# Kernel tuning notes

Hardware: AMD Instinct MI355X
Metric: run time of the kernel (lower is better)

Reference implementation:

```python
import jax, jax.numpy as jnp
import numpy as np

EPS = 1e-15
MAX_ATANH = 1.0 - 1e-5
V = 2097152   # total nodes (B*N*L flattened)
E = 8388608   # edges, ~avg degree 4 (temporal + parent/child)
ATT = 16
MAXD = 512    # mixer embedding table size
# curvature c = 1.0 (registered buffer, constant)


def _mobius_add(a, b):
    # Poincare ball Mobius addition, c = 1
    a2 = jnp.sum(a * a, -1, keepdims=True)
    b2 = jnp.sum(b * b, -1, keepdims=True)
    ab = jnp.sum(a * b, -1, keepdims=True)
    num = (1.0 + 2.0 * ab + b2) * a + (1.0 - a2) * b
    den = 1.0 + 2.0 * ab + a2 * b2
    return num / jnp.maximum(den, EPS)


def _log_map_x(x, y):
    # log_x(y): tangent vector at x pointing to y (c = 1)
    sub = _mobius_add(-x, y)
    n = jnp.maximum(jnp.linalg.norm(sub, axis=-1, keepdims=True), EPS)
    lam = 2.0 / jnp.maximum(1.0 - jnp.sum(x * x, -1, keepdims=True), EPS)
    return (2.0 / lam) * jnp.arctanh(jnp.minimum(n, MAX_ATANH)) * (sub / n)


def _exp_map_x(x, v):
    # exp_x(v) (c = 1)
    n = jnp.maximum(jnp.linalg.norm(v, axis=-1, keepdims=True), EPS)
    lam = 2.0 / jnp.maximum(1.0 - jnp.sum(x * x, -1, keepdims=True), EPS)
    return _mobius_add(x, jnp.tanh(0.5 * lam * n) * (v / n))


def setup_inputs() -> dict:
    key = jax.random.key(0)
    ks = jax.random.split(key, 8)
    # node embeddings strictly inside the unit ball: exp0 of a small tangent vec
    v0 = 0.5 * jax.random.normal(ks[0], (V, 2), jnp.float32)
    n0 = jnp.maximum(jnp.linalg.norm(v0, axis=-1, keepdims=True), EPS)
    x = jnp.tanh(n0) * v0 / n0
    edge_index = jax.random.randint(ks[1], (2, E), 0, V)
    depth = jax.random.randint(ks[2], (V,), 0, MAXD)
    W1 = jax.random.normal(ks[3], (2, ATT), jnp.float32) / jnp.sqrt(2.0)
    b1 = 0.1 * jax.random.normal(ks[4], (ATT,), jnp.float32)
    W2 = jax.random.normal(ks[5], (ATT, 1), jnp.float32) / jnp.sqrt(float(ATT))
    eta = jnp.float32(1.0)
    depth_scale = 1.0 + 0.01 * jax.random.normal(ks[6], (MAXD,), jnp.float32)
    depth_theta = 0.01 * jax.random.normal(ks[7], (MAXD,), jnp.float32)
    return {"x": x, "W1": W1, "b1": b1, "W2": W2, "eta": eta,
            "depth_scale": depth_scale, "depth_theta": depth_theta,
            "edge_index": edge_index, "depth": depth}


def reference(x, W1, b1, W2, eta, depth_scale, depth_theta, edge_index, depth):
    row, col = edge_index[0], edge_index[1]
    xi = x[row]                      # [E,2] gather target endpoints
    xj = x[col]                      # [E,2] gather source endpoints
    v_ij = _log_map_x(xi, xj)        # [E,2] hyperbolic log-map
    # small per-edge MLP scorer: Linear(2,16) -> GELU(exact) -> Linear(16,1)
    h = jax.nn.gelu(v_ij @ W1 + b1, approximate=False)
    scores = (h @ W2)[:, 0]          # [E]
    # segment softmax over target node (row)
    mx = jax.ops.segment_max(scores, row, num_segments=V)
    e = jnp.exp(scores - mx[row])
    den = jax.ops.segment_sum(e, row, num_segments=V)
    alpha = e / jnp.maximum(den[row], EPS)
    # scatter-add aggregate in tangent space
    m = jax.ops.segment_sum(alpha[:, None] * v_ij, row, num_segments=V)  # [V,2]
    # depth-gated mixer: per-node scale + 2D rotation
    d = jnp.minimum(depth, MAXD - 1)
    k = depth_scale[d][:, None]
    ang = depth_theta[d]
    ca, sa = jnp.cos(ang), jnp.sin(ang)
    m = k * jnp.stack([ca * m[:, 0] - sa * m[:, 1],
                       sa * m[:, 0] + ca * m[:, 1]], axis=-1)
    # exp-map update
    return _exp_map_x(x, eta * m)
```

## Files before the change

### kernel.cpp

```cpp
#include <hip/hip_runtime.h>
#include <math.h>

#define EPSF 1e-15f
#define MAX_ATANH (1.0f - 1e-5f)
#define ATT 16

#define LOG_NPB 11
#define NPB (1 << LOG_NPB)
#define MAXB 1024
#define NBLK 1024

__global__ void __launch_bounds__(256) hist_kernel(const int* __restrict__ row,
                                                   int E, int B,
                                                   unsigned* __restrict__ counts ) {
    __shared__ unsigned h[MAXB];
    for (int i = threadIdx.x; i < B; i += 256) h[i] = 0u;
    __syncthreads();
    const int T = gridDim.x * 256;
    for (int e = blockIdx.x * 256 + threadIdx.x; e < E; e += T)
        atomicAdd(&h[((unsigned)row[e]) >> LOG_NPB], 1u);
    __syncthreads();
    for (int i = threadIdx.x; i < B; i += 256)
        counts[(size_t)i * gridDim.x + blockIdx.x] = h[i];
}

__global__ void __launch_bounds__(256) scan_blocks_kernel(const unsigned* __restrict__ counts,
                                                          unsigned* __restrict__ within,
                                                          unsigned* __restrict__ totals,
                                                          int nblk) {
    const int b = blockIdx.x;
    const unsigned* src = counts + (size_t)b * nblk;
    unsigned* dst = within + (size_t)b * nblk;
    __shared__ unsigned s[256];
    const int ipt = (nblk + 255) / 256;
    unsigned vals[8];
    unsigned sum = 0u;
    for (int k = 0; k < ipt; ++k) {
        int idx = threadIdx.x * ipt + k;
        vals[k] = (idx < nblk) ? src[idx] : 0u;
        sum += vals[k];
    }
    s[threadIdx.x] = sum;
    __syncthreads();
    for (int off = 1; off < 256; off <<= 1) {
        unsigned t = (threadIdx.x >= off) ? s[threadIdx.x - off] : 0u;
        __syncthreads();
        s[threadIdx.x] += t;
        __syncthreads();
    }
    unsigned base = (threadIdx.x > 0) ? s[threadIdx.x - 1] : 0u;
    for (int k = 0; k < ipt; ++k) {
        int idx = threadIdx.x * ipt + k;
        if (idx < nblk) { dst[idx] = base; base += vals[k]; }
    }
    if (threadIdx.x == 255) totals[b] = s[255];
}

__global__ void __launch_bounds__(256) scan_totals_kernel(const unsigned* __restrict__ totals,
                                                          unsigned* __restrict__ base, int B) {
    __shared__ unsigned s[256];
    const int ipt = (B + 255) / 256;
    unsigned vals[8];
    unsigned sum = 0u;
    for (int k = 0; k < ipt; ++k) {
        int idx = threadIdx.x * ipt + k;
        vals[k] = (idx < B) ? totals[idx] : 0u;
        sum += vals[k];
    }
    s[threadIdx.x] = sum;
    __syncthreads();
    for (int off = 1; off < 256; off <<= 1) {
        unsigned t = (threadIdx.x >= off) ? s[threadIdx.x - off] : 0u;
        __syncthreads();
        s[threadIdx.x] += t;
        __syncthreads();
    }
    unsigned b0 = (threadIdx.x > 0) ? s[threadIdx.x - 1] : 0u;
    for (int k = 0; k < ipt; ++k) {
        int idx = threadIdx.x * ipt + k;
        if (idx < B) { base[idx] = b0; b0 += vals[k]; }
    }
    if (threadIdx.x == 255) base[B] = s[255];
}

__global__ void __launch_bounds__(256) scatter_kernel(const int* __restrict__ row,
                                                      const int* __restrict__ col,
                                                      int E, int B,
                                                      const unsigned* __restrict__ base,
                                                      const unsigned* __restrict__ within,
                                                      unsigned* __restrict__ payload) {
    __shared__ unsigned cur[MAXB];
    const int nblk = gridDim.x;
    for (int i = threadIdx.x; i < B; i += 256)
        cur[i] = base[i] + within[(size_t)i * nblk + blockIdx.x];
    __syncthreads();
    const int T = nblk * 256;
    for (int e = blockIdx.x * 256 + threadIdx.x; e < E; e += T) {
        const unsigned r = (unsigned)row[e];
        const unsigned b = r >> LOG_NPB;
        const unsigned pos = atomicAdd(&cur[b], 1u);
        payload[pos] = ((r & (NPB - 1)) << 21) | (unsigned)col[e];
    }
}

__global__ void __launch_bounds__(1024) bucket_reduce_kernel(
        const float2* __restrict__ x,
        const float* __restrict__ W1,
        const float* __restrict__ b1,
        const float* __restrict__ W2,
        const unsigned* __restrict__ base,
        const unsigned* __restrict__ payload,
        const int* __restrict__ depth,
        const float* __restrict__ depth_scale,
        const float* __restrict__ depth_theta,
        const float* __restrict__ eta_p,
        float2* __restrict__ out, int V) {
    __shared__ float sden[NPB];
    __shared__ float smx[NPB];
    __shared__ float smy[NPB];
    const int b = blockIdx.x;
    const int nodeBase = b << LOG_NPB;
    for (int i = threadIdx.x; i < NPB; i += blockDim.x) {
        sden[i] = 0.f; smx[i] = 0.f; smy[i] = 0.f;
    }
    __syncthreads();

    const unsigned e0 = base[b], e1 = base[b + 1];
    for (unsigned e = e0 + threadIdx.x; e < e1; e += blockDim.x) {
        const unsigned p = payload[e];
        const unsigned lrow = p >> 21;
        const unsigned c = p & 0x1FFFFFu;
        const float2 xi = x[nodeBase + (int)lrow];
        const float2 xj = x[c];

        const float ax = -xi.x, ay = -xi.y;
        const float bx = xj.x,  by = xj.y;
        const float a2 = ax * ax + ay * ay;
        const float b2 = bx * bx + by * by;
        const float ab = ax * bx + ay * by;
        const float ca = 1.0f + 2.0f * ab + b2;
        const float cb = 1.0f - a2;
        const float dn = fmaxf(1.0f + 2.0f * ab + a2 * b2, EPSF);
        const float subx = (ca * ax + cb * bx) / dn;
        const float suby = (ca * ay + cb * by) / dn;

        const float n = fmaxf(sqrtf(subx * subx + suby * suby), EPSF);
        const float M = fmaxf(1.0f - (xi.x * xi.x + xi.y * xi.y), EPSF);
        const float scl = M * atanhf(fminf(n, MAX_ATANH)) / n;
        const float vx = scl * subx;
        const float vy = scl * suby;

        float s = 0.0f;
        #pragma unroll
        for (int k = 0; k < ATT; ++k) {
            const float u = fmaf(vx, W1[k], fmaf(vy, W1[ATT + k], b1[k]));
            const float hk = 0.5f * u * (1.0f + erff(u * 0.70710678118654752f));
            s = fmaf(hk, W2[k], s);
        }

        const float ee = expf(s);
        atomicAdd(&sden[lrow], ee);
        atomicAdd(&smx[lrow], ee * vx);
        atomicAdd(&smy[lrow], ee * vy);
    }
    __syncthreads();

    const float eta = eta_p[0];
    for (int i = threadIdx.x; i < NPB; i += blockDim.x) {
        const int v = nodeBase + i;
        if (v >= V) break;
        const float dv = fmaxf(sden[i], EPSF);
        const float mx = smx[i] / dv;
        const float my = smy[i] / dv;

        const int d = min(depth[v], 511);
        const float k   = depth_scale[d];
        const float ang = depth_theta[d];
        const float cs = cosf(ang), sn = sinf(ang);
        const float m0 = eta * (k * (cs * mx - sn * my));
        const float m1 = eta * (k * (sn * mx + cs * my));

        const float2 xi = x[v];

        const float n = fmaxf(sqrtf(m0 * m0 + m1 * m1), EPSF);
        const float M = fmaxf(1.0f - (xi.x * xi.x + xi.y * xi.y), EPSF);
        const float t = tanhf(n / M);
        const float bx = t * m0 / n;
        const float by = t * m1 / n;

        const float a2 = xi.x * xi.x + xi.y * xi.y;
        const float b2 = bx * bx + by * by;
        const float ab = xi.x * bx + xi.y * by;
        const float ca = 1.0f + 2.0f * ab + b2;
        const float cb = 1.0f - a2;
        const float dn = fmaxf(1.0f + 2.0f * ab + a2 * b2, EPSF);

        out[v] = make_float2((ca * xi.x + cb * bx) / dn,
                             (ca * xi.y + cb * by) / dn);
    }
}

extern "C" void kernel_launch(void* const* d_in, const int* in_sizes, int n_in,
                              void* d_out, int out_size, void* d_ws, size_t ws_size,
                              hipStream_t stream) {
    const float2* x          = (const float2*)d_in[0];
    const float*  W1         = (const float*)d_in[1];
    const float*  b1         = (const float*)d_in[2];
    const float*  W2         = (const float*)d_in[3];
    const float*  eta        = (const float*)d_in[4];
    const float*  dscale     = (const float*)d_in[5];
    const float*  dtheta     = (const float*)d_in[6];
    const int*    edge_index = (const int*)d_in[7];
    const int*    depth      = (const int*)d_in[8];

    const int V = in_sizes[0] / 2;
    const int E = in_sizes[7] / 2;
    const int B = (V + NPB - 1) >> LOG_NPB;

    const int* row = edge_index;
    const int* col = edge_index + E;

    unsigned* payload = (unsigned*)d_ws;
    unsigned* counts  = payload + E;
    unsigned* within  = counts + (size_t)B * NBLK;
    unsigned* totals  = within + (size_t)B * NBLK;
    unsigned* base    = totals + B;

    hist_kernel<<<NBLK, 256, 0, stream>>>(row, E, B, counts);
    scan_blocks_kernel<<<B, 256, 0, stream>>>(counts, within, totals, NBLK);
    scan_totals_kernel<<<1, 256, 0, stream>>>(totals, base, B);
    scatter_kernel<<<NBLK, 256, 0, stream>>>(row, col, E, B, base, within, payload);
    bucket_reduce_kernel<<<B, 1024, 0, stream>>>(x, W1, b1, W2, base, payload,
                                                 depth, dscale, dtheta, eta,
                                                 (float2*)d_out, V);
}
```

Measured before the change: 303.3 us.

## Use fast intrinsic math for GELU/atanh/tanh and vectorize histogram/scatter loads

Replaces exact erff with an Abramowitz-Stegun polynomial GELU, and replaces atanhf, tanhf, expf, sin/cos and divisions with fast intrinsics and reciprocal multiplies in the per-edge and per-node math. The histogram and scatter kernels now read row/col as int4 vectors, and the scan kernels use uint4 loads specialized to NBLK. This cuts the transcendental-heavy ALU cost in the edge loop, at the price of lower numerical accuracy that may approach tolerance limits.

```diff
diff --git a/kernel.cpp b/kernel.cpp
--- a/kernel.cpp
+++ b/kernel.cpp
@@ -9,6 +9,28 @@
 #define NPB (1 << LOG_NPB)
 #define MAXB 1024
 #define NBLK 1024
+
+__device__ __forceinline__ float fast_gelu(float u) {
+    const float x  = fabsf(u) * 0.70710678118654752f;
+    const float w  = __fdividef(1.0f, fmaf(0.3275911f, x, 1.0f));
+    float p = 1.061405429f;
+    p = fmaf(p, w, -1.453152027f);
+    p = fmaf(p, w,  1.421413741f);
+    p = fmaf(p, w, -0.284496736f);
+    p = fmaf(p, w,  0.254829592f);
+    const float e    = __expf(-0.5f * u * u);
+    const float erfp = fmaf(-p * w, e, 1.0f);
+    const float er   = copysignf(erfp, u);
+    return 0.5f * u * (1.0f + er);
+}
+
+__device__ __forceinline__ float fast_atanh(float z) {
+    return 0.5f * __logf(__fdividef(1.0f + z, 1.0f - z));
+}
+
+__device__ __forceinline__ float fast_tanh(float z) {
+    return 1.0f - __fdividef(2.0f, __expf(2.0f * z) + 1.0f);
+}
 
 __global__ void __launch_bounds__(256) hist_kernel(const int* __restrict__ row,
                                                    int E, int B,
@@ -17,7 +39,16 @@
     for (int i = threadIdx.x; i < B; i += 256) h[i] = 0u;
     __syncthreads();
     const int T = gridDim.x * 256;
-    for (int e = blockIdx.x * 256 + threadIdx.x; e < E; e += T)
+    const int nv = E >> 2;
+    const int4* row4 = (const int4*)row;
+    for (int i = blockIdx.x * 256 + threadIdx.x; i < nv; i += T) {
+        const int4 r = row4[i];
+        atomicAdd(&h[((unsigned)r.x) >> LOG_NPB], 1u);
+        atomicAdd(&h[((unsigned)r.y) >> LOG_NPB], 1u);
+        atomicAdd(&h[((unsigned)r.z) >> LOG_NPB], 1u);
+        atomicAdd(&h[((unsigned)r.w) >> LOG_NPB], 1u);
+    }
+    for (int e = (nv << 2) + blockIdx.x * 256 + threadIdx.x; e < E; e += T)
         atomicAdd(&h[((unsigned)row[e]) >> LOG_NPB], 1u);
     __syncthreads();
     for (int i = threadIdx.x; i < B; i += 256)
@@ -26,21 +57,17 @@
 
 __global__ void __launch_bounds__(256) scan_blocks_kernel(const unsigned* __restrict__ counts,
                                                           unsigned* __restrict__ within,
-                                                          unsigned* __restrict__ totals,
-                                                          int nblk) {
+                                                          unsigned* __restrict__ totals) {
     const int b = blockIdx.x;
-    const unsigned* src = counts + (size_t)b * nblk;
-    unsigned* dst = within + (size_t)b * nblk;
+    const unsigned* src = counts + (size_t)b * NBLK;
+    unsigned* dst = within + (size_t)b * NBLK;
     __shared__ unsigned s[256];
-    const int ipt = (nblk + 255) / 256;
-    unsigned vals[8];
-    unsigned sum = 0u;
-    for (int k = 0; k < ipt; ++k) {
-        int idx = threadIdx.x * ipt + k;
-        vals[k] = (idx < nblk) ? src[idx] : 0u;
-        sum += vals[k];
-    }
-    s[threadIdx.x] = sum;
+    unsigned v0, v1, v2, v3;
+    {
+        const uint4 v = ((const uint4*)src)[threadIdx.x];
+        v0 = v.x; v1 = v.y; v2 = v.z; v3 = v.w;
+    }
+    s[threadIdx.x] = v0 + v1 + v2 + v3;
     __syncthreads();
     for (int off = 1; off < 256; off <<= 1) {
         unsigned t = (threadIdx.x >= off) ? s[threadIdx.x - off] : 0u;
@@ -49,25 +76,27 @@
         __syncthreads();
     }
     unsigned base = (threadIdx.x > 0) ? s[threadIdx.x - 1] : 0u;
-    for (int k = 0; k < ipt; ++k) {
-        int idx = threadIdx.x * ipt + k;
-        if (idx < nblk) { dst[idx] = base; base += vals[k]; }
-    }
+    uint4 o;
+    o.x = base; o.y = o.x + v0; o.z = o.y + v1; o.w = o.z + v2;
+    ((uint4*)dst)[threadIdx.x] = o;
     if (threadIdx.x == 255) totals[b] = s[255];
 }
 
 __global__ void __launch_bounds__(256) scan_totals_kernel(const unsigned* __restrict__ totals,
                                                           unsigned* __restrict__ base, int B) {
     __shared__ unsigned s[256];
-    const int ipt = (B + 255) / 256;
-    unsigned vals[8];
-    unsigned sum = 0u;
-    for (int k = 0; k < ipt; ++k) {
-        int idx = threadIdx.x * ipt + k;
-        vals[k] = (idx < B) ? totals[idx] : 0u;
-        sum += vals[k];
-    }
-    s[threadIdx.x] = sum;
+    unsigned v0 = 0, v1 = 0, v2 = 0, v3 = 0;
+    const int i0 = threadIdx.x * 4;
+    if (i0 + 3 < B) {
+        const uint4 v = ((const uint4*)totals)[threadIdx.x];
+        v0 = v.x; v1 = v.y; v2 = v.z; v3 = v.w;
+    } else {
+        if (i0 + 0 < B) v0 = totals[i0 + 0];
+        if (i0 + 1 < B) v1 = totals[i0 + 1];
+        if (i0 + 2 < B) v2 = totals[i0 + 2];
+        if (i0 + 3 < B) v3 = totals[i0 + 3];
+    }
+    s[threadIdx.x] = v0 + v1 + v2 + v3;
     __syncthreads();
     for (int off = 1; off < 256; off <<= 1) {
         unsigned t = (threadIdx.x >= off) ? s[threadIdx.x - off] : 0u;
@@ -76,10 +105,10 @@
         __syncthreads();
     }
     unsigned b0 = (threadIdx.x > 0) ? s[threadIdx.x - 1] : 0u;
-    for (int k = 0; k < ipt; ++k) {
-        int idx = threadIdx.x * ipt + k;
-        if (idx < B) { base[idx] = b0; b0 += vals[k]; }
-    }
+    if (i0 + 0 < B) base[i0 + 0] = b0;           b0 += v0;
+    if (i0 + 1 < B) base[i0 + 1] = b0;           b0 += v1;
+    if (i0 + 2 < B) base[i0 + 2] = b0;           b0 += v2;
+    if (i0 + 3 < B) base[i0 + 3] = b0;           b0 += v3;
     if (threadIdx.x == 255) base[B] = s[255];
 }
 
@@ -95,11 +124,37 @@
         cur[i] = base[i] + within[(size_t)i * nblk + blockIdx.x];
     __syncthreads();
     const int T = nblk * 256;
-    for (int e = blockIdx.x * 256 + threadIdx.x; e < E; e += T) {
-        const unsigned r = (unsigned)row[e];
-        const unsigned b = r >> LOG_NPB;
-        const unsigned pos = atomicAdd(&cur[b], 1u);
-        payload[pos] = ((r & (NPB - 1)) << 21) | (unsigned)col[e];
+    const int nv = E >> 2;
+    const int4* row4 = (const int4*)row;
+    const int4* col4 = (const int4*)col;
+    for (int i = blockIdx.x * 256 + threadIdx.x; i < nv; i += T) {
+        const int4 r = row4[i];
+        const int4 c = col4[i];
+        {
+            const unsigned rr = (unsigned)r.x;
+            const unsigned pos = atomicAdd(&cur[rr >> LOG_NPB], 1u);
+            payload[pos] = ((rr & (NPB - 1)) << 21) | (unsigned)c.x;
+        }
+        {
+            const unsigned rr = (unsigned)r.y;
+            const unsigned pos = atomicAdd(&cur[rr >> LOG_NPB], 1u);
+            payload[pos] = ((rr & (NPB - 1)) << 21) | (unsigned)c.y;
+        }
+        {
+            const unsigned rr = (unsigned)r.z;
+            const unsigned pos = atomicAdd(&cur[rr >> LOG_NPB], 1u);
+            payload[pos] = ((rr & (NPB - 1)) << 21) | (unsigned)c.z;
+        }
+        {
+            const unsigned rr = (unsigned)r.w;
+            const unsigned pos = atomicAdd(&cur[rr >> LOG_NPB], 1u);
+            payload[pos] = ((rr & (NPB - 1)) << 21) | (unsigned)c.w;
+        }
+    }
+    for (int e = (nv << 2) + blockIdx.x * 256 + threadIdx.x; e < E; e += T) {
+        const unsigned rr = (unsigned)row[e];
+        const unsigned pos = atomicAdd(&cur[rr >> LOG_NPB], 1u);
+        payload[pos] = ((rr & (NPB - 1)) << 21) | (unsigned)col[e];
     }
 }
 
@@ -141,12 +196,13 @@
         const float ca = 1.0f + 2.0f * ab + b2;
         const float cb = 1.0f - a2;
         const float dn = fmaxf(1.0f + 2.0f * ab + a2 * b2, EPSF);
-        const float subx = (ca * ax + cb * bx) / dn;
-        const float suby = (ca * ay + cb * by) / dn;
+        const float rdn = __fdividef(1.0f, dn);
+        const float subx = (ca * ax + cb * bx) * rdn;
+        const float suby = (ca * ay + cb * by) * rdn;
 
         const float n = fmaxf(sqrtf(subx * subx + suby * suby), EPSF);
         const float M = fmaxf(1.0f - (xi.x * xi.x + xi.y * xi.y), EPSF);
-        const float scl = M * atanhf(fminf(n, MAX_ATANH)) / n;
+        const float scl = M * fast_atanh(fminf(n, MAX_ATANH)) * __fdividef(1.0f, n);
         const float vx = scl * subx;
         const float vy = scl * suby;
 
@@ -154,11 +210,10 @@
         #pragma unroll
         for (int k = 0; k < ATT; ++k) {
             const float u = fmaf(vx, W1[k], fmaf(vy, W1[ATT + k], b1[k]));
-            const float hk = 0.5f * u * (1.0f + erff(u * 0.70710678118654752f));
-            s = fmaf(hk, W2[k], s);
-        }
-
-        const float ee = expf(s);
+            s = fmaf(fast_gelu(u), W2[k], s);
+        }
+
+        const float ee = __expf(s);
         atomicAdd(&sden[lrow], ee);
         atomicAdd(&smx[lrow], ee * vx);
         atomicAdd(&smy[lrow], ee * vy);
@@ -169,14 +224,14 @@
     for (int i = threadIdx.x; i < NPB; i += blockDim.x) {
         const int v = nodeBase + i;
         if (v >= V) break;
-        const float dv = fmaxf(sden[i], EPSF);
-        const float mx = smx[i] / dv;
-        const float my = smy[i] / dv;
+        const float rdv = __fdividef(1.0f, fmaxf(sden[i], EPSF));
+        const float mx = smx[i] * rdv;
+        const float my = smy[i] * rdv;
 
         const int d = min(depth[v], 511);
         const float k   = depth_scale[d];
         const float ang = depth_theta[d];
-        const float cs = cosf(ang), sn = sinf(ang);
+        const float cs = __cosf(ang), sn = __sinf(ang);
         const float m0 = eta * (k * (cs * mx - sn * my));
         const float m1 = eta * (k * (sn * mx + cs * my));
 
@@ -184,9 +239,10 @@
 
         const float n = fmaxf(sqrtf(m0 * m0 + m1 * m1), EPSF);
         const float M = fmaxf(1.0f - (xi.x * xi.x + xi.y * xi.y), EPSF);
-        const float t = tanhf(n / M);
-        const float bx = t * m0 / n;
-        const float by = t * m1 / n;
+        const float t = fast_tanh(__fdividef(n, M));
+        const float tn = t * __fdividef(1.0f, n);
+        const float bx = tn * m0;
+        const float by = tn * m1;
 
         const float a2 = xi.x * xi.x + xi.y * xi.y;
         const float b2 = bx * bx + by * by;
@@ -194,9 +250,10 @@
         const float ca = 1.0f + 2.0f * ab + b2;
         const float cb = 1.0f - a2;
         const float dn = fmaxf(1.0f + 2.0f * ab + a2 * b2, EPSF);
-
-        out[v] = make_float2((ca * xi.x + cb * bx) / dn,
-                             (ca * xi.y + cb * by) / dn);
+        const float rdn = __fdividef(1.0f, dn);
+
+        out[v] = make_float2((ca * xi.x + cb * bx) * rdn,
+                             (ca * xi.y + cb * by) * rdn);
     }
 }
 
@@ -227,7 +284,7 @@
     unsigned* base    = totals + B;
 
     hist_kernel<<<NBLK, 256, 0, stream>>>(row, E, B, counts);
-    scan_blocks_kernel<<<B, 256, 0, stream>>>(counts, within, totals, NBLK);
+    scan_blocks_kernel<<<B, 256, 0, stream>>>(counts, within, totals);
     scan_totals_kernel<<<1, 256, 0, stream>>>(totals, base, B);
     scatter_kernel<<<NBLK, 256, 0, stream>>>(row, col, E, B, base, within, payload);
     bucket_reduce_kernel<<<B, 1024, 0, stream>>>(x, W1, b1, W2, base, payload,
```

After: 285.6 us. 5.8% less time.
